# Kernel optimization log

Hardware: AMD Instinct MI355X
Metric: run time of the kernel (lower is better)

Reference implementation:

```python
import jax, jax.numpy as jnp
import numpy as np

N = 100_000      # nodes
E = 1_600_000    # edges (avg degree 16)
D = 64           # dim_node
H = 64           # dim_hidden
L = 4            # model_layer
G = 512          # num graphs
BN_EPS = 1e-5


def setup_inputs() -> dict:
    key = jax.random.key(0)
    ks = jax.random.split(key, 16)
    x = jax.random.normal(ks[0], (N, D), dtype=jnp.float32)
    edge_index = jax.random.randint(ks[1], (2, E), 0, N, dtype=jnp.int64)
    batch = jnp.sort(jax.random.randint(ks[2], (N,), 0, G, dtype=jnp.int64))
    s = 0.05
    # stacked per-layer params (all layers same shape since D == H)
    W1 = jax.random.normal(ks[3], (L, D, 2 * H), dtype=jnp.float32) * s
    b1 = jax.random.normal(ks[4], (L, 2 * H), dtype=jnp.float32) * s
    g1 = 1.0 + jax.random.normal(ks[5], (L, 2 * H), dtype=jnp.float32) * 0.1
    bt1 = jax.random.normal(ks[6], (L, 2 * H), dtype=jnp.float32) * 0.1
    m1 = jax.random.normal(ks[7], (L, 2 * H), dtype=jnp.float32) * 0.1
    v1 = jax.random.uniform(ks[8], (L, 2 * H), dtype=jnp.float32, minval=0.5, maxval=1.5)
    W2 = jax.random.normal(ks[9], (L, 2 * H, H), dtype=jnp.float32) * s
    b2 = jax.random.normal(ks[10], (L, H), dtype=jnp.float32) * s
    g2 = 1.0 + jax.random.normal(ks[11], (L, H), dtype=jnp.float32) * 0.1
    bt2 = jax.random.normal(ks[12], (L, H), dtype=jnp.float32) * 0.1
    m2 = jax.random.normal(ks[13], (L, H), dtype=jnp.float32) * 0.1
    v2 = jax.random.uniform(ks[14], (L, H), dtype=jnp.float32, minval=0.5, maxval=1.5)
    return {"x": x, "edge_index": edge_index, "batch": batch,
            "W1": W1, "b1": b1, "g1": g1, "bt1": bt1, "m1": m1, "v1": v1,
            "W2": W2, "b2": b2, "g2": g2, "bt2": bt2, "m2": m2, "v2": v2}


def _bn(h, m, v, g, b):
    # inference-mode BatchNorm1d with running stats
    return (h - m) * jax.lax.rsqrt(v + BN_EPS) * g + b


def reference(x, edge_index, batch, W1, b1, g1, bt1, m1, v1, W2, b2, g2, bt2, m2, v2):
    src, dst = edge_index[0], edge_index[1]
    h = x
    for i in range(L):
        # GINConv with eps=0: nn(x + sum_{j in N(i)} x_j)
        agg = jax.ops.segment_sum(h[src], dst, num_segments=N)  # [N, d]
        z = h + agg
        z = z @ W1[i] + b1[i]                 # [N, 2H]
        z = jax.nn.relu(_bn(z, m1[i], v1[i], g1[i], bt1[i]))
        z = z @ W2[i] + b2[i]                 # [N, H]
        z = _bn(z, m2[i], v2[i], g2[i], bt2[i])  # outer BatchNorm
        if i != L - 1:                        # ReLU skipped on final layer
            z = jax.nn.relu(z)
        # dropout = identity in eval mode
        h = z
    # global mean pool per graph
    sums = jax.ops.segment_sum(h, batch, num_segments=G)                    # [G, H]
    cnts = jax.ops.segment_sum(jnp.ones((N, 1), h.dtype), batch, num_segments=G)
    return sums / jnp.maximum(cnts, 1.0)
```

## Files before the change

kernel.cpp:

```cpp
#include <hip/hip_runtime.h>
#include <hip/hip_bf16.h>

#define N_NODES 100000
#define N_EDGES 1600000
#define N_GRAPHS 512
#define BN_EPS 1e-5f
#define NBLK_SCAN ((N_NODES + 255) / 256)
#define BM 128
#define NB_MLP ((N_NODES + BM - 1) / BM)
#define CB_SHIFT 9
#define NCB ((N_NODES + 511) / 512)
#define FB_EPB 4096
#define FB_BLOCKS ((N_EDGES + FB_EPB - 1) / FB_EPB)
#define SEG_CAP 11264

typedef short v8s __attribute__((ext_vector_type(8)));
typedef float v4f __attribute__((ext_vector_type(4)));

__device__ __forceinline__ unsigned short f2bf(float f) {
    union { float f; unsigned int i; } c; c.f = f;
    unsigned int lsb = (c.i >> 16) & 1;
    unsigned int r = c.i + 0x7FFFu + lsb;
    return (unsigned short)(r >> 16);
}
__device__ __forceinline__ float bflo(unsigned int u) {
    union { unsigned int i; float f; } c; c.i = u << 16; return c.f;
}
__device__ __forceinline__ float bfhi(unsigned int u) {
    union { unsigned int i; float f; } c; c.i = u & 0xFFFF0000u; return c.f;
}
__device__ __forceinline__ unsigned int packbf(float a, float b) {
    return (unsigned int)f2bf(a) | ((unsigned int)f2bf(b) << 16);
}
__device__ __forceinline__ int clampn(int v) {
    return v < 0 ? 0 : (v >= N_NODES ? N_NODES - 1 : v);
}

__global__ void convert_kernel(const float4* __restrict__ x, uint2* __restrict__ xb, int n16) {
    int i = blockIdx.x * blockDim.x + threadIdx.x;
    if (i < n16) {
        float4 a = x[i];
        uint2 u;
        u.x = packbf(a.x, a.y);
        u.y = packbf(a.z, a.w);
        xb[i] = u;
    }
}

__global__ void zero_int_kernel(int* __restrict__ p, int n) {
    int i = blockIdx.x * blockDim.x + threadIdx.x;
    if (i < n) p[i] = 0;
}

__global__ void hist_kernel(const int* __restrict__ ei, int* __restrict__ cnt) {
    int e = blockIdx.x * blockDim.x + threadIdx.x;
    if (e < N_EDGES) atomicAdd(&cnt[clampn(ei[N_EDGES + e])], 1);
}

__global__ void scanA_kernel(const int* __restrict__ cnt, int* __restrict__ bsum) {
    __shared__ int sc[256];
    int t = threadIdx.x;
    int idx = blockIdx.x * 256 + t;
    sc[t] = (idx < N_NODES) ? cnt[idx] : 0;
    __syncthreads();
    for (int off = 128; off > 0; off >>= 1) {
        if (t < off) sc[t] += sc[t + off];
        __syncthreads();
    }
    if (t == 0) bsum[blockIdx.x] = sc[0];
}

__global__ void scanB_kernel(const int* __restrict__ bsum, int* __restrict__ boff) {
    __shared__ int sb[NBLK_SCAN];
    int t = threadIdx.x;
    for (int i = t; i < NBLK_SCAN; i += blockDim.x) sb[i] = bsum[i];
    __syncthreads();
    if (t == 0) {
        int run = 0;
        for (int i = 0; i < NBLK_SCAN; ++i) { int v = sb[i]; sb[i] = run; run += v; }
    }
    __syncthreads();
    for (int i = t; i < NBLK_SCAN; i += blockDim.x) boff[i] = sb[i];
}

__global__ void scanC_kernel(const int* __restrict__ cnt, const int* __restrict__ boff,
                             int* __restrict__ row_start, int* __restrict__ cursor) {
    __shared__ int sc[256];
    int t = threadIdx.x;
    int idx = blockIdx.x * 256 + t;
    int v = (idx < N_NODES) ? cnt[idx] : 0;
    sc[t] = v;
    __syncthreads();
    for (int off = 1; off < 256; off <<= 1) {
        int add = (t >= off) ? sc[t - off] : 0;
        __syncthreads();
        sc[t] += add;
        __syncthreads();
    }
    if (idx < N_NODES) {
        int rs = boff[blockIdx.x] + sc[t] - v;
        row_start[idx] = rs;
        cursor[idx] = rs;
    }
    if (idx == 0) row_start[N_NODES] = N_EDGES;
}

__global__ void bucket_init_kernel(const int* __restrict__ row_start, int* __restrict__ gcur) {
    int b = blockIdx.x * blockDim.x + threadIdx.x;
    if (b < NCB) gcur[b] = row_start[b << CB_SHIFT];
}

__launch_bounds__(256)
__global__ void binfill_kernel(const int* __restrict__ ei, int* __restrict__ gcur,
                               unsigned int* __restrict__ bpk) {
    __shared__ int cnt[NCB];
    __shared__ int gbase[NCB];
    __shared__ int lcur[NCB];
    int tid = threadIdx.x;
    int e0 = blockIdx.x * FB_EPB;
    int e1 = e0 + FB_EPB;
    if (e1 > N_EDGES) e1 = N_EDGES;

    for (int b = tid; b < NCB; b += 256) cnt[b] = 0;
    __syncthreads();
    for (int e = e0 + tid; e < e1; e += 256) {
        int d = clampn(ei[N_EDGES + e]);
        atomicAdd(&cnt[d >> CB_SHIFT], 1);
    }
    __syncthreads();
    for (int b = tid; b < NCB; b += 256) {
        int c = cnt[b];
        gbase[b] = (c > 0) ? atomicAdd(&gcur[b], c) : 0;
        lcur[b] = 0;
    }
    __syncthreads();
    for (int e = e0 + tid; e < e1; e += 256) {
        int s = clampn(ei[e]);
        int d = clampn(ei[N_EDGES + e]);
        int b = d >> CB_SHIFT;
        int lpos = atomicAdd(&lcur[b], 1);
        bpk[gbase[b] + lpos] = ((unsigned int)s << CB_SHIFT) | (unsigned int)(d & 511);
    }
}

__launch_bounds__(256)
__global__ void binscatter_kernel(const unsigned int* __restrict__ bpk,
                                  const int* __restrict__ row_start,
                                  int* __restrict__ gcursor,
                                  int* __restrict__ adj) {
    __shared__ int seg[SEG_CAP];
    __shared__ int cur[1 << CB_SHIFT];

    int b = blockIdx.x;
    int tid = threadIdx.x;
    int nlo = b << CB_SHIFT;
    int nhi = nlo + (1 << CB_SHIFT);
    if (nhi > N_NODES) nhi = N_NODES;
    int base = row_start[nlo];
    int cnt  = row_start[nhi] - base;

    if (cnt <= SEG_CAP) {
        for (int i = nlo + tid; i < nhi; i += 256) cur[i - nlo] = row_start[i] - base;
        __syncthreads();
        for (int e = tid; e < cnt; e += 256) {
            unsigned int u = bpk[base + e];
            int pos = atomicAdd(&cur[u & 511u], 1);
            seg[pos] = (int)(u >> CB_SHIFT);
        }
        __syncthreads();
        for (int i = tid; i < cnt; i += 256) adj[base + i] = seg[i];
    } else {
        for (int e = tid; e < cnt; e += 256) {
            unsigned int u = bpk[base + e];
            int d = nlo + (int)(u & 511u);
            int pos = atomicAdd(&gcursor[d], 1);
            adj[pos] = (int)(u >> CB_SHIFT);
        }
    }
}

#define GATHER_BLOCKS 2048
__global__ void gather_kernel(const unsigned short* __restrict__ hin,
                              unsigned short* __restrict__ zb,
                              const int* __restrict__ row_start,
                              const int* __restrict__ adj) {
    const unsigned int* hu = (const unsigned int*)hin;
    unsigned int* zu = (unsigned int*)zb;
    const int j2 = threadIdx.x & 31;
    const int unit = (blockIdx.x * blockDim.x + threadIdx.x) >> 5;
    const int nunits = (gridDim.x * blockDim.x) >> 5;

    for (int n = unit; n < N_NODES; n += nunits) {
        int beg = row_start[n];
        int end = row_start[n + 1];
        unsigned int us = hu[(size_t)n * 32 + j2];
        float s0 = bflo(us), s1 = bfhi(us);

        int i = beg;
        for (; i + 8 <= end; i += 8) {
            int a0 = adj[i],     a1 = adj[i + 1], a2 = adj[i + 2], a3 = adj[i + 3];
            int a4 = adj[i + 4], a5 = adj[i + 5], a6 = adj[i + 6], a7 = adj[i + 7];
            unsigned int u0 = hu[(size_t)a0 * 32 + j2];
            unsigned int u1 = hu[(size_t)a1 * 32 + j2];
            unsigned int u2 = hu[(size_t)a2 * 32 + j2];
            unsigned int u3 = hu[(size_t)a3 * 32 + j2];
            unsigned int u4 = hu[(size_t)a4 * 32 + j2];
            unsigned int u5 = hu[(size_t)a5 * 32 + j2];
            unsigned int u6 = hu[(size_t)a6 * 32 + j2];
            unsigned int u7 = hu[(size_t)a7 * 32 + j2];
            s0 += ((bflo(u0) + bflo(u1)) + (bflo(u2) + bflo(u3)))
                + ((bflo(u4) + bflo(u5)) + (bflo(u6) + bflo(u7)));
            s1 += ((bfhi(u0) + bfhi(u1)) + (bfhi(u2) + bfhi(u3)))
                + ((bfhi(u4) + bfhi(u5)) + (bfhi(u6) + bfhi(u7)));
        }
        if (i + 4 <= end) {
            int a0 = adj[i], a1 = adj[i + 1], a2 = adj[i + 2], a3 = adj[i + 3];
            unsigned int u0 = hu[(size_t)a0 * 32 + j2];
            unsigned int u1 = hu[(size_t)a1 * 32 + j2];
            unsigned int u2 = hu[(size_t)a2 * 32 + j2];
            unsigned int u3 = hu[(size_t)a3 * 32 + j2];
            s0 += (bflo(u0) + bflo(u1)) + (bflo(u2) + bflo(u3));
            s1 += (bfhi(u0) + bfhi(u1)) + (bfhi(u2) + bfhi(u3));
            i += 4;
        }
        if (i + 2 <= end) {
            int a0 = adj[i], a1 = adj[i + 1];
            unsigned int u0 = hu[(size_t)a0 * 32 + j2];
            unsigned int u1 = hu[(size_t)a1 * 32 + j2];
            s0 += bflo(u0) + bflo(u1);
            s1 += bfhi(u0) + bfhi(u1);
            i += 2;
        }
        if (i < end) {
            unsigned int u0 = hu[(size_t)adj[i] * 32 + j2];
            s0 += bflo(u0);
            s1 += bfhi(u0);
        }

        zu[(size_t)n * 32 + j2] = packbf(s0, s1);
    }
}

__launch_bounds__(256)
__global__ void mlp_mfma_kernel(const unsigned short* __restrict__ zg,
                                unsigned short* __restrict__ hb,
                                const float* __restrict__ W1, const float* __restrict__ b1,
                                const float* __restrict__ g1, const float* __restrict__ bt1,
                                const float* __restrict__ m1, const float* __restrict__ v1,
                                const float* __restrict__ W2, const float* __restrict__ b2,
                                const float* __restrict__ g2, const float* __restrict__ bt2,
                                const float* __restrict__ m2, const float* __restrict__ v2,
                                int relu_out) {
    __shared__ __align__(16) char smem[53760];
    float* s1p = (float*)(smem);
    float* o1p = (float*)(smem + 512);
    float* o2p = (float*)(smem + 1024);
    float* s2p = (float*)(smem + 1280);
    short* tb  = (short*)(smem + 1536);
    short* w1b = (short*)(smem + 1536);
    short* w2b = (short*)(smem + 36352);

    const int tid = threadIdx.x;
    const int nbase = blockIdx.x * BM;

    if (tid < 128) {
        float sv = g1[tid] * rsqrtf(v1[tid] + BN_EPS);
        s1p[tid] = sv;
        o1p[tid] = (b1[tid] - m1[tid]) * sv + bt1[tid];
    } else if (tid < 192) {
        int j = tid - 128;
        float sv = g2[j] * rsqrtf(v2[j] + BN_EPS);
        s2p[j] = sv;
        o2p[j] = (b2[j] - m2[j]) * sv + bt2[j];
    }
    __syncthreads();

    {
        int n = tid & 127;
        int kc = tid >> 7;
        float sv = s1p[n];
        for (int k = kc * 32; k < kc * 32 + 32; k += 2) {
            float w0 = W1[k * 128 + n] * sv;
            float w1 = W1[(k + 1) * 128 + n] * sv;
            unsigned int u = (unsigned int)f2bf(w0) | ((unsigned int)f2bf(w1) << 16);
            *(unsigned int*)(w1b + n * 72 + k) = u;
        }
    }
    {
        int jo = tid & 63;
        int c = tid >> 6;
        float sv = s2p[jo];
        for (int jh = c * 32; jh < c * 32 + 32; jh += 2) {
            float w0 = W2[jh * 64 + jo] * sv;
            float w1 = W2[(jh + 1) * 64 + jo] * sv;
            unsigned int u = (unsigned int)f2bf(w0) | ((unsigned int)f2bf(w1) << 16);
            *(unsigned int*)(w2b + jo * 136 + jh) = u;
        }
    }
    __syncthreads();

    const int wave = tid >> 6;
    const int lane = tid & 63;
    const int lr = lane & 15;
    const int quad = lane >> 4;
    const int m0 = wave * 32;

    int ra0 = nbase + m0 + lr;       ra0 = ra0 < N_NODES ? ra0 : N_NODES - 1;
    int ra1 = nbase + m0 + 16 + lr;  ra1 = ra1 < N_NODES ? ra1 : N_NODES - 1;
    const v8s* pa0 = (const v8s*)(zg + (size_t)ra0 * 64 + quad * 8);
    const v8s* pa1 = (const v8s*)(zg + (size_t)ra1 * 64 + quad * 8);
    v8s a0k[2], a1k[2];
    a0k[0] = pa0[0]; a0k[1] = pa0[4];
    a1k[0] = pa1[0]; a1k[1] = pa1[4];

    v4f acc1[2][8];
    #pragma unroll
    for (int rt = 0; rt < 2; ++rt)
        #pragma unroll
        for (int ct = 0; ct < 8; ++ct)
            acc1[rt][ct] = (v4f){0.f, 0.f, 0.f, 0.f};

    #pragma unroll
    for (int ks = 0; ks < 2; ++ks) {
        int kb = ks * 32 + quad * 8;
        #pragma unroll
        for (int ct = 0; ct < 8; ++ct) {
            v8s bF = *(const v8s*)(w1b + (ct * 16 + lr) * 72 + kb);
            acc1[0][ct] = __builtin_amdgcn_mfma_f32_16x16x32_bf16(a0k[ks], bF, acc1[0][ct], 0, 0, 0);
            acc1[1][ct] = __builtin_amdgcn_mfma_f32_16x16x32_bf16(a1k[ks], bF, acc1[1][ct], 0, 0, 0);
        }
    }

    __syncthreads();

    #pragma unroll
    for (int rt = 0; rt < 2; ++rt) {
        #pragma unroll
        for (int ct = 0; ct < 8; ++ct) {
            int col = ct * 16 + lr;
            float o1v = o1p[col];
            #pragma unroll
            for (int r = 0; r < 4; ++r) {
                float v = acc1[rt][ct][r] + o1v;
                v = fmaxf(v, 0.0f);
                int row = m0 + rt * 16 + quad * 4 + r;
                tb[row * 136 + col] = (short)f2bf(v);
            }
        }
    }

    v4f acc2[2][4];
    #pragma unroll
    for (int rt = 0; rt < 2; ++rt)
        #pragma unroll
        for (int ct = 0; ct < 4; ++ct)
            acc2[rt][ct] = (v4f){0.f, 0.f, 0.f, 0.f};

    #pragma unroll
    for (int ks = 0; ks < 4; ++ks) {
        int kb = ks * 32 + quad * 8;
        v8s a0 = *(const v8s*)(tb + (m0 + lr) * 136 + kb);
        v8s a1 = *(const v8s*)(tb + (m0 + 16 + lr) * 136 + kb);
        #pragma unroll
        for (int ct = 0; ct < 4; ++ct) {
            v8s bF = *(const v8s*)(w2b + (ct * 16 + lr) * 136 + kb);
            acc2[0][ct] = __builtin_amdgcn_mfma_f32_16x16x32_bf16(a0, bF, acc2[0][ct], 0, 0, 0);
            acc2[1][ct] = __builtin_amdgcn_mfma_f32_16x16x32_bf16(a1, bF, acc2[1][ct], 0, 0, 0);
        }
    }

    #pragma unroll
    for (int rt = 0; rt < 2; ++rt) {
        #pragma unroll
        for (int ct = 0; ct < 4; ++ct) {
            int col = ct * 16 + lr;
            float o2v = o2p[col];
            #pragma unroll
            for (int r = 0; r < 4; ++r) {
                int row = m0 + rt * 16 + quad * 4 + r;
                int n = nbase + row;
                if (n < N_NODES) {
                    float v = acc2[rt][ct][r] + o2v;
                    if (relu_out) v = fmaxf(v, 0.0f);
                    hb[(size_t)n * 64 + col] = f2bf(v);
                }
            }
        }
    }
}

__launch_bounds__(256)
__global__ void pool_kernel(const unsigned short* __restrict__ hb,
                            const int* __restrict__ batch,
                            float* __restrict__ out) {
    __shared__ float part[4][64];
    int g = blockIdx.x;
    int tid = threadIdx.x;
    int w = tid >> 6;
    int j = tid & 63;

    int lo = 0, hi = N_NODES;
    while (lo < hi) { int mid = (lo + hi) >> 1; if (batch[mid] < g) lo = mid + 1; else hi = mid; }
    int start = lo;
    hi = N_NODES;
    while (lo < hi) { int mid = (lo + hi) >> 1; if (batch[mid] < g + 1) lo = mid + 1; else hi = mid; }
    int end = lo;

    float sum = 0.0f;
    int n = start + w;
    for (; n + 4 < end; n += 8) {
        unsigned int ua = (unsigned int)hb[(size_t)n * 64 + j];
        unsigned int ub = (unsigned int)hb[(size_t)(n + 4) * 64 + j];
        union { unsigned int i; float f; } ca, cb;
        ca.i = ua << 16; cb.i = ub << 16;
        sum += ca.f + cb.f;
    }
    if (n < end) {
        unsigned int u = (unsigned int)hb[(size_t)n * 64 + j];
        union { unsigned int i; float f; } c; c.i = u << 16;
        sum += c.f;
    }
    part[w][j] = sum;
    __syncthreads();
    if (w == 0) {
        float s = (part[0][j] + part[1][j]) + (part[2][j] + part[3][j]);
        float cnt = (float)(end - start);
        out[g * 64 + j] = s / fmaxf(cnt, 1.0f);
    }
}

extern "C" void kernel_launch(void* const* d_in, const int* in_sizes, int n_in,
                              void* d_out, int out_size, void* d_ws, size_t ws_size,
                              hipStream_t stream) {
    const float* x   = (const float*)d_in[0];
    const int* ei    = (const int*)d_in[1];
    const int* batch = (const int*)d_in[2];
    const float* W1  = (const float*)d_in[3];
    const float* b1  = (const float*)d_in[4];
    const float* g1  = (const float*)d_in[5];
    const float* bt1 = (const float*)d_in[6];
    const float* m1  = (const float*)d_in[7];
    const float* v1  = (const float*)d_in[8];
    const float* W2  = (const float*)d_in[9];
    const float* b2  = (const float*)d_in[10];
    const float* g2  = (const float*)d_in[11];
    const float* bt2 = (const float*)d_in[12];
    const float* m2  = (const float*)d_in[13];
    const float* v2  = (const float*)d_in[14];

    unsigned short* hb = (unsigned short*)d_ws;
    unsigned short* xb = hb + (size_t)N_NODES * 64;
    unsigned short* zb = xb + (size_t)N_NODES * 64;
    int* cnt       = (int*)(zb + (size_t)N_NODES * 64);
    int* row_start = cnt + N_NODES;
    int* cursor    = row_start + N_NODES + 1;
    int* adj       = cursor + N_NODES;
    int* bsum      = adj + N_EDGES;
    int* boff      = bsum + NBLK_SCAN;
    int* gcur      = boff + NBLK_SCAN;
    unsigned int* bpk = (unsigned int*)(gcur + NCB);

    float* out = (float*)d_out;

    const int EB = (N_EDGES + 255) / 256;

    const int n16 = N_NODES * 16;
    convert_kernel<<<(n16 + 255) / 256, 256, 0, stream>>>((const float4*)x, (uint2*)xb, n16);

    zero_int_kernel<<<NBLK_SCAN, 256, 0, stream>>>(cnt, N_NODES);
    hist_kernel<<<EB, 256, 0, stream>>>(ei, cnt);
    scanA_kernel<<<NBLK_SCAN, 256, 0, stream>>>(cnt, bsum);
    scanB_kernel<<<1, 512, 0, stream>>>(bsum, boff);
    scanC_kernel<<<NBLK_SCAN, 256, 0, stream>>>(cnt, boff, row_start, cursor);
    bucket_init_kernel<<<1, 256, 0, stream>>>(row_start, gcur);
    binfill_kernel<<<FB_BLOCKS, 256, 0, stream>>>(ei, gcur, bpk);
    binscatter_kernel<<<NCB, 256, 0, stream>>>(bpk, row_start, cursor, adj);

    for (int l = 0; l < 4; ++l) {
        const unsigned short* hin = (l == 0) ? xb : hb;
        gather_kernel<<<GATHER_BLOCKS, 256, 0, stream>>>(hin, zb, row_start, adj);
        mlp_mfma_kernel<<<NB_MLP, 256, 0, stream>>>(
            zb, hb,
            W1 + (size_t)l * 64 * 128, b1 + l * 128, g1 + l * 128, bt1 + l * 128,
            m1 + l * 128, v1 + l * 128,
            W2 + (size_t)l * 128 * 64, b2 + l * 64, g2 + l * 64, bt2 + l * 64,
            m2 + l * 64, v2 + l * 64,
            (l != 3) ? 1 : 0);
    }

    pool_kernel<<<N_GRAPHS, 256, 0, stream>>>(hb, batch, out);
}
```

Before: 431.8 us.

## Build CSR from coarse bucket histogram and compute per-node offsets inside binscatter

Replaces the full per-node global-atomic histogram and three-kernel scan with a coarse 512-node bucket histogram built in shared memory, plus a single small scan. Per-node counts and exclusive prefix offsets are now computed in shared memory inside binscatter, which also writes row_start. This removes 1.6M global atomics and several kernel launches from the CSR build. In exchange binscatter reads its bucket twice and runs a block-level scan.

```diff
diff --git a/kernel.cpp b/kernel.cpp
--- a/kernel.cpp
+++ b/kernel.cpp
@@ -5,7 +5,6 @@
 #define N_EDGES 1600000
 #define N_GRAPHS 512
 #define BN_EPS 1e-5f
-#define NBLK_SCAN ((N_NODES + 255) / 256)
 #define BM 128
 #define NB_MLP ((N_NODES + BM - 1) / BM)
 #define CB_SHIFT 9
@@ -47,67 +46,40 @@
     }
 }
 
-__global__ void zero_int_kernel(int* __restrict__ p, int n) {
+__global__ void zero_small_kernel(int* __restrict__ p, int n) {
     int i = blockIdx.x * blockDim.x + threadIdx.x;
     if (i < n) p[i] = 0;
 }
 
-__global__ void hist_kernel(const int* __restrict__ ei, int* __restrict__ cnt) {
-    int e = blockIdx.x * blockDim.x + threadIdx.x;
-    if (e < N_EDGES) atomicAdd(&cnt[clampn(ei[N_EDGES + e])], 1);
-}
-
-__global__ void scanA_kernel(const int* __restrict__ cnt, int* __restrict__ bsum) {
-    __shared__ int sc[256];
-    int t = threadIdx.x;
-    int idx = blockIdx.x * 256 + t;
-    sc[t] = (idx < N_NODES) ? cnt[idx] : 0;
-    __syncthreads();
-    for (int off = 128; off > 0; off >>= 1) {
-        if (t < off) sc[t] += sc[t + off];
-        __syncthreads();
-    }
-    if (t == 0) bsum[blockIdx.x] = sc[0];
-}
-
-__global__ void scanB_kernel(const int* __restrict__ bsum, int* __restrict__ boff) {
-    __shared__ int sb[NBLK_SCAN];
-    int t = threadIdx.x;
-    for (int i = t; i < NBLK_SCAN; i += blockDim.x) sb[i] = bsum[i];
-    __syncthreads();
-    if (t == 0) {
+__launch_bounds__(256)
+__global__ void cbhist_kernel(const int* __restrict__ ei, int* __restrict__ cbcnt) {
+    __shared__ int h[NCB];
+    int tid = threadIdx.x;
+    for (int b = tid; b < NCB; b += 256) h[b] = 0;
+    __syncthreads();
+    int e0 = blockIdx.x * FB_EPB;
+    int e1 = e0 + FB_EPB;
+    if (e1 > N_EDGES) e1 = N_EDGES;
+    for (int e = e0 + tid; e < e1; e += 256)
+        atomicAdd(&h[clampn(ei[N_EDGES + e]) >> CB_SHIFT], 1);
+    __syncthreads();
+    for (int b = tid; b < NCB; b += 256)
+        if (h[b] > 0) atomicAdd(&cbcnt[b], h[b]);
+}
+
+__global__ void cbscan_kernel(const int* __restrict__ cbcnt,
+                              int* __restrict__ bucket_base, int* __restrict__ gcur) {
+    __shared__ int s[NCB];
+    int tid = threadIdx.x;
+    for (int i = tid; i < NCB; i += 256) s[i] = cbcnt[i];
+    __syncthreads();
+    if (tid == 0) {
         int run = 0;
-        for (int i = 0; i < NBLK_SCAN; ++i) { int v = sb[i]; sb[i] = run; run += v; }
-    }
-    __syncthreads();
-    for (int i = t; i < NBLK_SCAN; i += blockDim.x) boff[i] = sb[i];
-}
-
-__global__ void scanC_kernel(const int* __restrict__ cnt, const int* __restrict__ boff,
-                             int* __restrict__ row_start, int* __restrict__ cursor) {
-    __shared__ int sc[256];
-    int t = threadIdx.x;
-    int idx = blockIdx.x * 256 + t;
-    int v = (idx < N_NODES) ? cnt[idx] : 0;
-    sc[t] = v;
-    __syncthreads();
-    for (int off = 1; off < 256; off <<= 1) {
-        int add = (t >= off) ? sc[t - off] : 0;
-        __syncthreads();
-        sc[t] += add;
-        __syncthreads();
-    }
-    if (idx < N_NODES) {
-        int rs = boff[blockIdx.x] + sc[t] - v;
-        row_start[idx] = rs;
-        cursor[idx] = rs;
-    }
-    if (idx == 0) row_start[N_NODES] = N_EDGES;
-}
-
-__global__ void bucket_init_kernel(const int* __restrict__ row_start, int* __restrict__ gcur) {
-    int b = blockIdx.x * blockDim.x + threadIdx.x;
-    if (b < NCB) gcur[b] = row_start[b << CB_SHIFT];
+        for (int i = 0; i < NCB; ++i) { int v = s[i]; s[i] = run; run += v; }
+    }
+    __syncthreads();
+    for (int i = tid; i < NCB; i += 256) { bucket_base[i] = s[i]; gcur[i] = s[i]; }
+    if (tid == 0) bucket_base[NCB] = N_EDGES;
 }
 
 __launch_bounds__(256)
@@ -145,26 +117,50 @@
 
 __launch_bounds__(256)
 __global__ void binscatter_kernel(const unsigned int* __restrict__ bpk,
-                                  const int* __restrict__ row_start,
-                                  int* __restrict__ gcursor,
+                                  const int* __restrict__ bucket_base,
+                                  int* __restrict__ row_start,
                                   int* __restrict__ adj) {
     __shared__ int seg[SEG_CAP];
-    __shared__ int cur[1 << CB_SHIFT];
+    __shared__ int lcnt[512];
+    __shared__ int lpre[512];
 
     int b = blockIdx.x;
     int tid = threadIdx.x;
     int nlo = b << CB_SHIFT;
-    int nhi = nlo + (1 << CB_SHIFT);
-    if (nhi > N_NODES) nhi = N_NODES;
-    int base = row_start[nlo];
-    int cnt  = row_start[nhi] - base;
+    int nn = N_NODES - nlo; if (nn > 512) nn = 512;
+    int base = bucket_base[b];
+    int cnt  = bucket_base[b + 1] - base;
+
+    lcnt[tid] = 0; lcnt[tid + 256] = 0;
+    __syncthreads();
+    for (int e = tid; e < cnt; e += 256)
+        atomicAdd(&lcnt[bpk[base + e] & 511u], 1);
+    __syncthreads();
+    int i0 = tid, i1 = tid + 256;
+    lpre[i0] = lcnt[i0]; lpre[i1] = lcnt[i1];
+    __syncthreads();
+    for (int st = 1; st < 512; st <<= 1) {
+        int v0 = (i0 >= st) ? lpre[i0 - st] : 0;
+        int v1 = (i1 >= st) ? lpre[i1 - st] : 0;
+        __syncthreads();
+        lpre[i0] += v0; lpre[i1] += v1;
+        __syncthreads();
+    }
+    {
+        int ex0 = lpre[i0] - lcnt[i0];
+        int ex1 = lpre[i1] - lcnt[i1];
+        if (i0 < nn) row_start[nlo + i0] = base + ex0;
+        if (i1 < nn) row_start[nlo + i1] = base + ex1;
+        lcnt[i0] = ex0;
+        lcnt[i1] = ex1;
+    }
+    if (b == NCB - 1 && tid == 0) row_start[N_NODES] = N_EDGES;
+    __syncthreads();
 
     if (cnt <= SEG_CAP) {
-        for (int i = nlo + tid; i < nhi; i += 256) cur[i - nlo] = row_start[i] - base;
-        __syncthreads();
         for (int e = tid; e < cnt; e += 256) {
             unsigned int u = bpk[base + e];
-            int pos = atomicAdd(&cur[u & 511u], 1);
+            int pos = atomicAdd(&lcnt[u & 511u], 1);
             seg[pos] = (int)(u >> CB_SHIFT);
         }
         __syncthreads();
@@ -172,9 +168,8 @@
     } else {
         for (int e = tid; e < cnt; e += 256) {
             unsigned int u = bpk[base + e];
-            int d = nlo + (int)(u & 511u);
-            int pos = atomicAdd(&gcursor[d], 1);
-            adj[pos] = (int)(u >> CB_SHIFT);
+            int pos = atomicAdd(&lcnt[u & 511u], 1);
+            adj[base + pos] = (int)(u >> CB_SHIFT);
         }
     }
 }
@@ -451,30 +446,23 @@
     unsigned short* hb = (unsigned short*)d_ws;
     unsigned short* xb = hb + (size_t)N_NODES * 64;
     unsigned short* zb = xb + (size_t)N_NODES * 64;
-    int* cnt       = (int*)(zb + (size_t)N_NODES * 64);
-    int* row_start = cnt + N_NODES;
-    int* cursor    = row_start + N_NODES + 1;
-    int* adj       = cursor + N_NODES;
-    int* bsum      = adj + N_EDGES;
-    int* boff      = bsum + NBLK_SCAN;
-    int* gcur      = boff + NBLK_SCAN;
+    int* row_start = (int*)(zb + (size_t)N_NODES * 64);
+    int* adj       = row_start + N_NODES + 1;
+    int* cbcnt     = adj + N_EDGES;
+    int* bucket_base = cbcnt + NCB;
+    int* gcur      = bucket_base + NCB + 1;
     unsigned int* bpk = (unsigned int*)(gcur + NCB);
 
     float* out = (float*)d_out;
-
-    const int EB = (N_EDGES + 255) / 256;
 
     const int n16 = N_NODES * 16;
     convert_kernel<<<(n16 + 255) / 256, 256, 0, stream>>>((const float4*)x, (uint2*)xb, n16);
 
-    zero_int_kernel<<<NBLK_SCAN, 256, 0, stream>>>(cnt, N_NODES);
-    hist_kernel<<<EB, 256, 0, stream>>>(ei, cnt);
-    scanA_kernel<<<NBLK_SCAN, 256, 0, stream>>>(cnt, bsum);
-    scanB_kernel<<<1, 512, 0, stream>>>(bsum, boff);
-    scanC_kernel<<<NBLK_SCAN, 256, 0, stream>>>(cnt, boff, row_start, cursor);
-    bucket_init_kernel<<<1, 256, 0, stream>>>(row_start, gcur);
+    zero_small_kernel<<<1, 256, 0, stream>>>(cbcnt, NCB);
+    cbhist_kernel<<<FB_BLOCKS, 256, 0, stream>>>(ei, cbcnt);
+    cbscan_kernel<<<1, 256, 0, stream>>>(cbcnt, bucket_base, gcur);
     binfill_kernel<<<FB_BLOCKS, 256, 0, stream>>>(ei, gcur, bpk);
-    binscatter_kernel<<<NCB, 256, 0, stream>>>(bpk, row_start, cursor, adj);
+    binscatter_kernel<<<NCB, 256, 0, stream>>>(bpk, bucket_base, row_start, adj);
 
     for (int l = 0; l < 4; ++l) {
         const unsigned short* hin = (l == 0) ? xb : hb;
```

Result: faster. 376.3 us (-12.9%).
